# Kernel optimization log

Measured on AMD Instinct MI355X. Metric: run time of the kernel, lower is better.

## Reference

```python
import jax, jax.numpy as jnp
import numpy as np

RADIUS = 0.3      # extents/2, extents = radius_scale*6*particle_radius = 4*6*0.025 = 0.6
KSIZE = 4         # kernel_size [4,4,4]
KMAX = 80         # padded neighbor count
N = 50000
BOX = 5.2         # box side -> ~40 neighbors within RADIUS on average
CIN = 3
COUT = 3
_PI = 3.14159265358979323846


def _build_neighbors(pos, radius, kmax):
    # fixed-radius search (L2), ignore_query_point=True, padded to kmax per row
    n = pos.shape[0]
    r2 = radius * radius
    sq = (pos * pos).sum(1)
    idx = np.zeros((n, kmax), np.int32)
    msk = np.zeros((n, kmax), np.bool_)
    ch = 2500
    for s in range(0, n, ch):
        e = min(s + ch, n)
        d2 = sq[s:e, None] + sq[None, :] - 2.0 * (pos[s:e] @ pos.T)
        d2[np.arange(e - s), np.arange(s, e)] = np.inf  # radius_search_ignore_query_points
        rows, cols = np.nonzero(d2 < r2)
        starts = np.searchsorted(rows, np.arange(e - s))
        slot = np.arange(len(rows)) - starts[rows]
        keep = slot < kmax
        idx[rows[keep] + s, slot[keep]] = cols[keep]
        msk[rows[keep] + s, slot[keep]] = True
    return idx, msk


def setup_inputs():
    key = jax.random.key(0)
    k1, k2, k3 = jax.random.split(key, 3)
    pos = jax.random.uniform(k1, (N, 3), jnp.float32) * BOX
    vel = jax.random.normal(k2, (N, 3), jnp.float32)
    # keras 'uniform' initializer: U(-0.05, 0.05)
    kernel = jax.random.uniform(k3, (KSIZE, KSIZE, KSIZE, CIN, COUT), jnp.float32, -0.05, 0.05)
    nidx, nmask = _build_neighbors(np.asarray(pos), RADIUS, KMAX)
    return {"pos": pos, "vel": vel, "kernel": kernel,
            "neighbor_idx": jnp.asarray(nidx), "neighbor_mask": jnp.asarray(nmask)}


def _ball_to_cube_volume_preserving(u):
    # Open3D CoordinateTransformation.h: MapSphereToCylinder then MapCylinderToCube
    eps = 1e-12
    x, y, z = u[..., 0], u[..., 1], u[..., 2]
    sq = x * x + y * y + z * z
    norm = jnp.sqrt(jnp.maximum(sq, eps))
    sq_xy = x * x + y * y
    # sphere -> cylinder
    top = (1.25 * z * z) > sq_xy
    s_top = jnp.sqrt(3.0 * norm / (norm + jnp.abs(z)))
    s_side = norm / jnp.sqrt(jnp.maximum(sq_xy, eps))
    x1 = jnp.where(top, x * s_top, x * s_side)
    y1 = jnp.where(top, y * s_top, y * s_side)
    z1 = jnp.where(top, jnp.sign(z) * norm, 1.5 * z)
    small = sq < eps
    x1 = jnp.where(small, x, x1)
    y1 = jnp.where(small, y, y1)
    z1 = jnp.where(small, z, z1)
    # cylinder -> cube (equal-area disc->square on xy)
    sq_xy1 = x1 * x1 + y1 * y1
    norm_xy = jnp.sqrt(jnp.maximum(sq_xy1, eps))
    xbig = jnp.abs(y1) <= jnp.abs(x1)
    sx = jnp.sign(x1) * norm_xy
    sy = jnp.sign(y1) * norm_xy
    safe_x = jnp.where(jnp.abs(x1) > eps, x1, 1.0)
    safe_y = jnp.where(jnp.abs(y1) > eps, y1, 1.0)
    x2 = jnp.where(xbig, sx, sy * (4.0 / _PI) * jnp.arctan(x1 / safe_y))
    y2 = jnp.where(xbig, sx * (4.0 / _PI) * jnp.arctan(y1 / safe_x), sy)
    small_xy = sq_xy1 < eps
    x2 = jnp.where(small_xy, x1, x2)
    y2 = jnp.where(small_xy, y1, y2)
    return x2, y2, z1


def _grid_coords(c):
    # align_corners=True: [-1,1] -> [0, KSIZE-1]; 'linear' interpolation clamps to border
    t = jnp.clip((c + 1.0) * (0.5 * (KSIZE - 1)), 0.0, KSIZE - 1.0)
    t0 = jnp.floor(t)
    i0 = t0.astype(jnp.int32)
    i1 = jnp.minimum(i0 + 1, KSIZE - 1)
    f = t - t0
    return (i0, i1), (1.0 - f, f)


def _cconv(pos, vel, kernel, neighbor_idx, neighbor_mask):
    n = pos.shape[0]
    rel = pos[neighbor_idx] - pos[:, None, :]              # [N,K,3]
    d2 = jnp.sum(rel * rel, -1)
    # window_poly6 on squared distance normalized by radius^2
    imp = jnp.clip((1.0 - d2 / (RADIUS * RADIUS)) ** 3, 0.0, 1.0)
    imp = imp * neighbor_mask.astype(vel.dtype)
    cx, cy, cz = _ball_to_cube_volume_preserving(rel / RADIUS)
    (xi0, xi1), (wx0, wx1) = _grid_coords(cx)
    (yi0, yi1), (wy0, wy1) = _grid_coords(cy)
    (zi0, zi1), (wz0, wz1) = _grid_coords(cz)
    phi = vel[neighbor_idx] * imp[..., None]               # [N,K,Cin]
    rows = jnp.arange(n)[:, None]
    # accumulate window*trilinear-weighted features into the 64 filter taps,
    # then contract once with the flattened kernel (math identical to per-pair
    # interp(W) @ feat since everything is linear)
    A = jnp.zeros((n, KSIZE * KSIZE * KSIZE, vel.shape[1]), vel.dtype)
    for zi, wz in ((zi0, wz0), (zi1, wz1)):
        for yi, wy in ((yi0, wy0), (yi1, wy1)):
            for xi, wx in ((xi0, wx0), (xi1, wx1)):
                corner = (zi * KSIZE + yi) * KSIZE + xi
                A = A.at[rows, corner].add((wz * wy * wx)[..., None] * phi)
    Wflat = kernel.reshape(KSIZE * KSIZE * KSIZE, kernel.shape[3], kernel.shape[4])
    return jnp.einsum('ngi,gio->no', A, Wflat)        # [N, COUT]


def reference(pos, vel, kernel, neighbor_idx, neighbor_mask):
    return _cconv(pos, vel, kernel, neighbor_idx, neighbor_mask)
```

## Files before the change

kernel.cpp:

```cpp
#include <hip/hip_runtime.h>
#include <math.h>

#define N_PART 50000
#define KMAX 80
#define KS 4
#define LPP 16

typedef __attribute__((ext_vector_type(8))) _Float16 h8;
typedef __attribute__((ext_vector_type(2))) _Float16 h2;

__device__ __forceinline__ float atan_poly(float t) {
    float t2 = t * t;
    float p = -0.01172120f;
    p = p * t2 + 0.05265332f;
    p = p * t2 - 0.11643287f;
    p = p * t2 + 0.19354346f;
    p = p * t2 - 0.33262347f;
    p = p * t2 + 0.99997726f;
    return t * p;
}

template <typename MT>
__device__ __forceinline__ int prefix_count(const MT* __restrict__ nmask, int base, int sub) {
    int lc = 0; bool more = true;
    #pragma unroll
    for (int i = 0; i < 5; ++i) {
        bool t = nmask[base + sub * 5 + i] != 0;
        lc += (more && t) ? 1 : 0;
        more = more && t;
    }
    bool full = (lc == 5);
    unsigned long long nb = __ballot(!full);
    int wl  = threadIdx.x & 63;
    int grp = wl >> 4;
    unsigned int gb = (unsigned int)((nb >> (16 * grp)) & 0xFFFFull);
    if (gb == 0) return KMAX;
    int fi  = __ffs(gb) - 1;
    int flc = __shfl(lc, (grp << 4) + fi, 64);
    return fi * 5 + flc;
}

struct PV { float px, py, pz, ux, uy, uz; };

__device__ __forceinline__ void load_pv(const float* __restrict__ pos,
                                        const float* __restrict__ vel,
                                        int i, PV& v) {
    v.px = pos[3*i];  v.py = pos[3*i+1];  v.pz = pos[3*i+2];
    v.ux = vel[3*i];  v.uy = vel[3*i+1];  v.uz = vel[3*i+2];
}

__device__ __forceinline__ void pair_contrib(
    const PV& n, float cpx, float cpy, float cpz, float vmask,
    const _Float16* __restrict__ WsH, const float* __restrict__ Ws8,
    float& acc0, float& acc1, float& acc2)
{
    const float inv_r = 1.0f / 0.3f;
    const float eps   = 1e-12f;
    const float FOUR_OVER_PI = 1.27323954473516268615f;

    float rx = (n.px - cpx) * inv_r;
    float ry = (n.py - cpy) * inv_r;
    float rz = (n.pz - cpz) * inv_r;

    float sq = rx * rx + ry * ry + rz * rz;

    float t1  = 1.0f - sq;
    float imp = fminf(fmaxf(t1 * t1 * t1, 0.0f), 1.0f) * vmask;

    float norm  = sqrtf(fmaxf(sq, eps));
    float sq_xy = rx * rx + ry * ry;
    bool  top   = (1.25f * rz * rz) > sq_xy;
    float s_top  = sqrtf(3.0f * norm * __builtin_amdgcn_rcpf(norm + fabsf(rz)));
    float s_side = norm * __builtin_amdgcn_rsqf(fmaxf(sq_xy, eps));
    float s  = top ? s_top : s_side;
    float x1 = rx * s;
    float y1 = ry * s;
    float z1 = top ? copysignf(norm, rz) : 1.5f * rz;
    if (sq < eps) { x1 = rx; y1 = ry; z1 = rz; }

    float sq1 = x1 * x1 + y1 * y1;
    float nxy = sqrtf(fmaxf(sq1, eps));
    bool  xb  = fabsf(y1) <= fabsf(x1);
    float num = xb ? y1 : x1;
    float den = xb ? x1 : y1;
    float sden = (fabsf(den) > eps) ? den : 1.0f;
    float t    = num * __builtin_amdgcn_rcpf(sden);
    float at   = atan_poly(t);
    float sd   = copysignf(nxy, den);
    float u    = sd * FOUR_OVER_PI * at;
    float x2   = xb ? sd : u;
    float y2   = xb ? u  : sd;
    if (sq1 < eps) { x2 = x1; y2 = y1; }

    float tx = fminf(fmaxf((x2 + 1.0f) * 1.5f, 0.0f), 3.0f);
    float ty = fminf(fmaxf((y2 + 1.0f) * 1.5f, 0.0f), 3.0f);
    float tz = fminf(fmaxf((z1 + 1.0f) * 1.5f, 0.0f), 3.0f);
    float fx0 = floorf(tx), fy0 = floorf(ty), fz0 = floorf(tz);
    int xi0 = (int)fx0, yi0 = (int)fy0, zi0 = (int)fz0;
    int xi1 = min(xi0 + 1, KS - 1);
    int yi1 = min(yi0 + 1, KS - 1);
    int zi1 = min(zi0 + 1, KS - 1);
    float wx1 = tx - fx0, wx0 = 1.0f - wx1;
    float wy1 = ty - fy0, wy0 = 1.0f - wy1;
    float wz1 = tz - fz0, wz0 = 1.0f - wz1;

    int   zia[2] = { zi0, zi1 };  float wza[2] = { wz0, wz1 };
    int   yia[2] = { yi0, yi1 };  float wya[2] = { wy0, wy1 };
    int   xia[2] = { xi0, xi1 };  float wxa[2] = { wx0, wx1 };

    h2 M01 = (h2)(_Float16)0.0f;
    h2 M23 = (h2)(_Float16)0.0f;
    h2 M45 = (h2)(_Float16)0.0f;
    h2 M67 = (h2)(_Float16)0.0f;
    float m8 = 0.0f;

    #pragma unroll
    for (int cz = 0; cz < 2; ++cz) {
        #pragma unroll
        for (int cy = 0; cy < 2; ++cy) {
            float wzy = wza[cz] * wya[cy];
            #pragma unroll
            for (int cx = 0; cx < 2; ++cx) {
                int corner = (zia[cz] * KS + yia[cy]) * KS + xia[cx];
                h8 wv = *(const h8*)&WsH[corner << 3];
                float wf = wzy * wxa[cx];
                _Float16 wh = (_Float16)wf;
                h2 ww = { wh, wh };
                M01 += ww * __builtin_shufflevector(wv, wv, 0, 1);
                M23 += ww * __builtin_shufflevector(wv, wv, 2, 3);
                M45 += ww * __builtin_shufflevector(wv, wv, 4, 5);
                M67 += ww * __builtin_shufflevector(wv, wv, 6, 7);
                m8  += wf * Ws8[corner];
            }
        }
    }

    float m0 = (float)M01[0], m1 = (float)M01[1];
    float m2 = (float)M23[0], m3 = (float)M23[1];
    float m4 = (float)M45[0], m5 = (float)M45[1];
    float m6 = (float)M67[0], m7 = (float)M67[1];
    float s0 = n.ux * m0 + n.uy * m3 + n.uz * m6;
    float s1 = n.ux * m1 + n.uy * m4 + n.uz * m7;
    float s2 = n.ux * m2 + n.uy * m5 + n.uz * m8;
    acc0 += imp * s0;
    acc1 += imp * s1;
    acc2 += imp * s2;
}

__global__ __launch_bounds__(256) void cconv_kernel(
    const float* __restrict__ pos,
    const float* __restrict__ vel,
    const float* __restrict__ Wg,
    const int* __restrict__ nidx,
    const void* __restrict__ nmask,
    float* __restrict__ out)
{
    __shared__ _Float16 WsH[64 * 8];
    __shared__ float    Ws8[64];
    for (int t = threadIdx.x; t < 64 * 8; t += blockDim.x) {
        int g = t >> 3, r = t & 7;
        WsH[t] = (_Float16)Wg[g * 9 + r];
    }
    for (int t = threadIdx.x; t < 64; t += blockDim.x)
        Ws8[t] = Wg[t * 9 + 8];
    __syncthreads();

    int gid = blockIdx.x * blockDim.x + threadIdx.x;
    int p   = gid >> 4;
    int sub = gid & 15;
    if (p >= N_PART) return;

    const int base = p * KMAX;

    int idxs[5];
    #pragma unroll
    for (int m = 0; m < 5; ++m)
        idxs[m] = nidx[base + sub + (m << 4)];

    bool byteMask;
    {
        const unsigned* mw = (const unsigned*)nmask;
        int lane = threadIdx.x & 63;
        bool big = false;
        #pragma unroll
        for (int i = 0; i < 8; ++i)
            big |= (mw[lane + 64 * i] > 1u);
        byteMask = (__ballot(big) != 0ULL);
    }

    float cpx = pos[3 * p], cpy = pos[3 * p + 1], cpz = pos[3 * p + 2];

    int cnt;
    if (byteMask) cnt = prefix_count<unsigned char>((const unsigned char*)nmask, base, sub);
    else          cnt = prefix_count<int>((const int*)nmask, base, sub);

    int rem   = cnt - sub;
    int trips = (rem > 0) ? ((rem + 31) >> 5) : 0;

    PV A0, A1, A0n, A1n;
    load_pv(pos, vel, idxs[0], A0);
    load_pv(pos, vel, idxs[1], A1);

    float acc0 = 0.0f, acc1 = 0.0f, acc2 = 0.0f;

    for (int j = 0; j < trips; ++j) {
        int mn0 = min(2 * j + 2, 4);
        int mn1 = min(2 * j + 3, 4);
        load_pv(pos, vel, idxs[mn0], A0n);
        load_pv(pos, vel, idxs[mn1], A1n);

        int   k1 = sub + ((2 * j + 1) << 4);
        float v1 = (k1 < cnt) ? 1.0f : 0.0f;

        pair_contrib(A0, cpx, cpy, cpz, 1.0f, WsH, Ws8, acc0, acc1, acc2);
        pair_contrib(A1, cpx, cpy, cpz, v1,   WsH, Ws8, acc0, acc1, acc2);

        A0 = A0n; A1 = A1n;
    }

    acc0 += __shfl_xor(acc0, 1); acc0 += __shfl_xor(acc0, 2);
    acc0 += __shfl_xor(acc0, 4); acc0 += __shfl_xor(acc0, 8);
    acc1 += __shfl_xor(acc1, 1); acc1 += __shfl_xor(acc1, 2);
    acc1 += __shfl_xor(acc1, 4); acc1 += __shfl_xor(acc1, 8);
    acc2 += __shfl_xor(acc2, 1); acc2 += __shfl_xor(acc2, 2);
    acc2 += __shfl_xor(acc2, 4); acc2 += __shfl_xor(acc2, 8);

    if (sub == 0) {
        out[p * 3 + 0] = acc0;
        out[p * 3 + 1] = acc1;
        out[p * 3 + 2] = acc2;
    }
}

extern "C" void kernel_launch(void* const* d_in, const int* in_sizes, int n_in,
                              void* d_out, int out_size, void* d_ws, size_t ws_size,
                              hipStream_t stream) {
    const float* pos   = (const float*)d_in[0];
    const float* vel   = (const float*)d_in[1];
    const float* Wg    = (const float*)d_in[2];
    const int*   nidx  = (const int*)d_in[3];
    const void*  nmask = d_in[4];
    float*       out   = (float*)d_out;

    int threads = 256;
    long long total = (long long)N_PART * LPP;
    int grid = (int)((total + threads - 1) / threads);
    cconv_kernel<<<grid, threads, 0, stream>>>(pos, vel, Wg, nidx, nmask, out);
}
```

Measured before the change: 33.05 us.

## Parallelize over neighbor pairs with segmented wave reduction and atomics

Replaces the per-particle kernel (16 lanes looping over neighbors) with one thread per neighbor slot, reducing contributions per particle via a segmented shuffle scan within each wavefront and atomicAdd across wavefronts. A separate kernel zeroes the output first. This aims to expose more parallelism and drop the prefix-count loop, but it processes padded slots, adds a 6-step scan, atomics and an extra launch.

After: 51.25 us. +55.0%, slower.

```diff
diff --git a/kernel.cpp b/kernel.cpp
--- a/kernel.cpp
+++ b/kernel.cpp
@@ -4,7 +4,7 @@
 #define N_PART 50000
 #define KMAX 80
 #define KS 4
-#define LPP 16
+#define NTOT (N_PART * KMAX)
 
 typedef __attribute__((ext_vector_type(8))) _Float16 h8;
 typedef __attribute__((ext_vector_type(2))) _Float16 h2;
@@ -20,52 +20,69 @@
     return t * p;
 }
 
-template <typename MT>
-__device__ __forceinline__ int prefix_count(const MT* __restrict__ nmask, int base, int sub) {
-    int lc = 0; bool more = true;
-    #pragma unroll
-    for (int i = 0; i < 5; ++i) {
-        bool t = nmask[base + sub * 5 + i] != 0;
-        lc += (more && t) ? 1 : 0;
-        more = more && t;
-    }
-    bool full = (lc == 5);
-    unsigned long long nb = __ballot(!full);
-    int wl  = threadIdx.x & 63;
-    int grp = wl >> 4;
-    unsigned int gb = (unsigned int)((nb >> (16 * grp)) & 0xFFFFull);
-    if (gb == 0) return KMAX;
-    int fi  = __ffs(gb) - 1;
-    int flc = __shfl(lc, (grp << 4) + fi, 64);
-    return fi * 5 + flc;
-}
-
-struct PV { float px, py, pz, ux, uy, uz; };
-
-__device__ __forceinline__ void load_pv(const float* __restrict__ pos,
-                                        const float* __restrict__ vel,
-                                        int i, PV& v) {
-    v.px = pos[3*i];  v.py = pos[3*i+1];  v.pz = pos[3*i+2];
-    v.ux = vel[3*i];  v.uy = vel[3*i+1];  v.uz = vel[3*i+2];
-}
-
-__device__ __forceinline__ void pair_contrib(
-    const PV& n, float cpx, float cpy, float cpz, float vmask,
-    const _Float16* __restrict__ WsH, const float* __restrict__ Ws8,
-    float& acc0, float& acc1, float& acc2)
+__global__ __launch_bounds__(256) void zero_out_kernel(float* __restrict__ out, int n) {
+    int i = blockIdx.x * blockDim.x + threadIdx.x;
+    if (i < n) out[i] = 0.0f;
+}
+
+__global__ __launch_bounds__(256) void cconv_pair_kernel(
+    const float* __restrict__ pos,
+    const float* __restrict__ vel,
+    const float* __restrict__ Wg,
+    const int* __restrict__ nidx,
+    const void* __restrict__ nmask,
+    float* __restrict__ out)
 {
+    __shared__ _Float16 WsH[64 * 8];
+    __shared__ float    Ws8[64];
+    for (int t = threadIdx.x; t < 64 * 8; t += blockDim.x) {
+        int g = t >> 3, r = t & 7;
+        WsH[t] = (_Float16)Wg[g * 9 + r];
+    }
+    for (int t = threadIdx.x; t < 64; t += blockDim.x)
+        Ws8[t] = Wg[t * 9 + 8];
+    __syncthreads();
+
+    int t = blockIdx.x * blockDim.x + threadIdx.x;
+    unsigned tu = (unsigned)t;
+    int p    = (int)(tu / 80u);
+    int lane = threadIdx.x & 63;
+
+    bool byteMask;
+    {
+        const unsigned* mw = (const unsigned*)nmask;
+        bool big = false;
+        #pragma unroll
+        for (int i = 0; i < 8; ++i)
+            big |= (mw[lane + 64 * i] > 1u);
+        byteMask = (__ballot(big) != 0ULL);
+    }
+
+    bool valid;
+    if (byteMask) valid = ((const unsigned char*)nmask)[t] != 0;
+    else          valid = ((const int*)nmask)[t] != 0;
+
+    if (__ballot(valid) == 0ULL) return;
+
+    int   idx  = nidx[t];
+    float vmsk = valid ? 1.0f : 0.0f;
+
     const float inv_r = 1.0f / 0.3f;
     const float eps   = 1e-12f;
     const float FOUR_OVER_PI = 1.27323954473516268615f;
 
-    float rx = (n.px - cpx) * inv_r;
-    float ry = (n.py - cpy) * inv_r;
-    float rz = (n.pz - cpz) * inv_r;
+    float cpx = pos[3 * p], cpy = pos[3 * p + 1], cpz = pos[3 * p + 2];
+    float npx = pos[3 * idx], npy = pos[3 * idx + 1], npz = pos[3 * idx + 2];
+    float ux  = vel[3 * idx], uy  = vel[3 * idx + 1], uz  = vel[3 * idx + 2];
+
+    float rx = (npx - cpx) * inv_r;
+    float ry = (npy - cpy) * inv_r;
+    float rz = (npz - cpz) * inv_r;
 
     float sq = rx * rx + ry * ry + rz * rz;
 
     float t1  = 1.0f - sq;
-    float imp = fminf(fmaxf(t1 * t1 * t1, 0.0f), 1.0f) * vmask;
+    float imp = fminf(fmaxf(t1 * t1 * t1, 0.0f), 1.0f) * vmsk;
 
     float norm  = sqrtf(fmaxf(sq, eps));
     float sq_xy = rx * rx + ry * ry;
@@ -84,8 +101,8 @@
     float num = xb ? y1 : x1;
     float den = xb ? x1 : y1;
     float sden = (fabsf(den) > eps) ? den : 1.0f;
-    float t    = num * __builtin_amdgcn_rcpf(sden);
-    float at   = atan_poly(t);
+    float tt   = num * __builtin_amdgcn_rcpf(sden);
+    float at   = atan_poly(tt);
     float sd   = copysignf(nxy, den);
     float u    = sd * FOUR_OVER_PI * at;
     float x2   = xb ? sd : u;
@@ -139,96 +156,31 @@
     float m2 = (float)M23[0], m3 = (float)M23[1];
     float m4 = (float)M45[0], m5 = (float)M45[1];
     float m6 = (float)M67[0], m7 = (float)M67[1];
-    float s0 = n.ux * m0 + n.uy * m3 + n.uz * m6;
-    float s1 = n.ux * m1 + n.uy * m4 + n.uz * m7;
-    float s2 = n.ux * m2 + n.uy * m5 + n.uz * m8;
-    acc0 += imp * s0;
-    acc1 += imp * s1;
-    acc2 += imp * s2;
-}
-
-__global__ __launch_bounds__(256) void cconv_kernel(
-    const float* __restrict__ pos,
-    const float* __restrict__ vel,
-    const float* __restrict__ Wg,
-    const int* __restrict__ nidx,
-    const void* __restrict__ nmask,
-    float* __restrict__ out)
-{
-    __shared__ _Float16 WsH[64 * 8];
-    __shared__ float    Ws8[64];
-    for (int t = threadIdx.x; t < 64 * 8; t += blockDim.x) {
-        int g = t >> 3, r = t & 7;
-        WsH[t] = (_Float16)Wg[g * 9 + r];
-    }
-    for (int t = threadIdx.x; t < 64; t += blockDim.x)
-        Ws8[t] = Wg[t * 9 + 8];
-    __syncthreads();
-
-    int gid = blockIdx.x * blockDim.x + threadIdx.x;
-    int p   = gid >> 4;
-    int sub = gid & 15;
-    if (p >= N_PART) return;
-
-    const int base = p * KMAX;
-
-    int idxs[5];
+    float v0 = imp * (ux * m0 + uy * m3 + uz * m6);
+    float v1 = imp * (ux * m1 + uy * m4 + uz * m7);
+    float v2 = imp * (ux * m2 + uy * m5 + uz * m8);
+
     #pragma unroll
-    for (int m = 0; m < 5; ++m)
-        idxs[m] = nidx[base + sub + (m << 4)];
-
-    bool byteMask;
-    {
-        const unsigned* mw = (const unsigned*)nmask;
-        int lane = threadIdx.x & 63;
-        bool big = false;
-        #pragma unroll
-        for (int i = 0; i < 8; ++i)
-            big |= (mw[lane + 64 * i] > 1u);
-        byteMask = (__ballot(big) != 0ULL);
-    }
-
-    float cpx = pos[3 * p], cpy = pos[3 * p + 1], cpz = pos[3 * p + 2];
-
-    int cnt;
-    if (byteMask) cnt = prefix_count<unsigned char>((const unsigned char*)nmask, base, sub);
-    else          cnt = prefix_count<int>((const int*)nmask, base, sub);
-
-    int rem   = cnt - sub;
-    int trips = (rem > 0) ? ((rem + 31) >> 5) : 0;
-
-    PV A0, A1, A0n, A1n;
-    load_pv(pos, vel, idxs[0], A0);
-    load_pv(pos, vel, idxs[1], A1);
-
-    float acc0 = 0.0f, acc1 = 0.0f, acc2 = 0.0f;
-
-    for (int j = 0; j < trips; ++j) {
-        int mn0 = min(2 * j + 2, 4);
-        int mn1 = min(2 * j + 3, 4);
-        load_pv(pos, vel, idxs[mn0], A0n);
-        load_pv(pos, vel, idxs[mn1], A1n);
-
-        int   k1 = sub + ((2 * j + 1) << 4);
-        float v1 = (k1 < cnt) ? 1.0f : 0.0f;
-
-        pair_contrib(A0, cpx, cpy, cpz, 1.0f, WsH, Ws8, acc0, acc1, acc2);
-        pair_contrib(A1, cpx, cpy, cpz, v1,   WsH, Ws8, acc0, acc1, acc2);
-
-        A0 = A0n; A1 = A1n;
-    }
-
-    acc0 += __shfl_xor(acc0, 1); acc0 += __shfl_xor(acc0, 2);
-    acc0 += __shfl_xor(acc0, 4); acc0 += __shfl_xor(acc0, 8);
-    acc1 += __shfl_xor(acc1, 1); acc1 += __shfl_xor(acc1, 2);
-    acc1 += __shfl_xor(acc1, 4); acc1 += __shfl_xor(acc1, 8);
-    acc2 += __shfl_xor(acc2, 1); acc2 += __shfl_xor(acc2, 2);
-    acc2 += __shfl_xor(acc2, 4); acc2 += __shfl_xor(acc2, 8);
-
-    if (sub == 0) {
-        out[p * 3 + 0] = acc0;
-        out[p * 3 + 1] = acc1;
-        out[p * 3 + 2] = acc2;
+    for (int d = 1; d < 64; d <<= 1) {
+        int src = lane - d;
+        int cs  = max(src, 0);
+        int   pp = __shfl(p,  cs, 64);
+        float f0 = __shfl(v0, cs, 64);
+        float f1 = __shfl(v1, cs, 64);
+        float f2 = __shfl(v2, cs, 64);
+        bool take = (src >= 0) && (pp == p);
+        v0 += take ? f0 : 0.0f;
+        v1 += take ? f1 : 0.0f;
+        v2 += take ? f2 : 0.0f;
+    }
+
+    int  nl = min(lane + 1, 63);
+    int  pn = __shfl(p, nl, 64);
+    bool lastInSeg = (lane == 63) || (pn != p);
+    if (lastInSeg) {
+        atomicAdd(&out[3 * p + 0], v0);
+        atomicAdd(&out[3 * p + 1], v1);
+        atomicAdd(&out[3 * p + 2], v2);
     }
 }
 
@@ -242,8 +194,10 @@
     const void*  nmask = d_in[4];
     float*       out   = (float*)d_out;
 
+    int nOut = out_size;
+    zero_out_kernel<<<(nOut + 255) / 256, 256, 0, stream>>>(out, nOut);
+
     int threads = 256;
-    long long total = (long long)N_PART * LPP;
-    int grid = (int)((total + threads - 1) / threads);
-    cconv_kernel<<<grid, threads, 0, stream>>>(pos, vel, Wg, nidx, nmask, out);
-}
+    int grid    = NTOT / threads;
+    cconv_pair_kernel<<<grid, threads, 0, stream>>>(pos, vel, Wg, nidx, nmask, out);
+}
```

## Switch to persistent kernel with atomic work queues and simplify cylinder-norm math

Applied to the files above, without the earlier changes.

The kernel becomes persistent: 2048 blocks of waves pull quads of four particles from four partitioned atomic counters in the workspace, which is zeroed by a memset before launch. This is meant to balance uneven neighbor counts across waves and to cut block launch overhead. The weight staging into shared memory and the mask-format check now run once per wave instead of once per particle group. Separately, the cylinder radius nxy and the octant test are computed directly from existing values, dropping one sqrt and some arithmetic. The cost is an extra memset launch plus atomic traffic, and the ordering of work changes.

Measured after the change: 109.8 us. 3.32x slower.

```diff
diff --git a/kernel.cpp b/kernel.cpp
--- a/kernel.cpp
+++ b/kernel.cpp
@@ -4,7 +4,8 @@
 #define N_PART 50000
 #define KMAX 80
 #define KS 4
-#define LPP 16
+#define NQUAD 12500
+#define QPC 3125
 
 typedef __attribute__((ext_vector_type(8))) _Float16 h8;
 typedef __attribute__((ext_vector_type(2))) _Float16 h2;
@@ -67,22 +68,23 @@
     float t1  = 1.0f - sq;
     float imp = fminf(fmaxf(t1 * t1 * t1, 0.0f), 1.0f) * vmask;
 
-    float norm  = sqrtf(fmaxf(sq, eps));
-    float sq_xy = rx * rx + ry * ry;
-    bool  top   = (1.25f * rz * rz) > sq_xy;
+    float norm   = sqrtf(fmaxf(sq, eps));
+    float sq_xy  = rx * rx + ry * ry;
+    bool  top    = (1.25f * rz * rz) > sq_xy;
+    float rsq_xy = __builtin_amdgcn_rsqf(fmaxf(sq_xy, eps));
     float s_top  = sqrtf(3.0f * norm * __builtin_amdgcn_rcpf(norm + fabsf(rz)));
-    float s_side = norm * __builtin_amdgcn_rsqf(fmaxf(sq_xy, eps));
+    float s_side = norm * rsq_xy;
     float s  = top ? s_top : s_side;
     float x1 = rx * s;
     float y1 = ry * s;
     float z1 = top ? copysignf(norm, rz) : 1.5f * rz;
     if (sq < eps) { x1 = rx; y1 = ry; z1 = rz; }
 
-    float sq1 = x1 * x1 + y1 * y1;
-    float nxy = sqrtf(fmaxf(sq1, eps));
-    bool  xb  = fabsf(y1) <= fabsf(x1);
-    float num = xb ? y1 : x1;
-    float den = xb ? x1 : y1;
+    float nxy = top ? (sq_xy * rsq_xy * s_top) : norm;
+    float sq1 = nxy * nxy;
+    bool  xb  = fabsf(ry) <= fabsf(rx);
+    float num = xb ? ry : rx;
+    float den = xb ? rx : ry;
     float sden = (fabsf(den) > eps) ? den : 1.0f;
     float t    = num * __builtin_amdgcn_rcpf(sden);
     float at   = atan_poly(t);
@@ -147,12 +149,13 @@
     acc2 += imp * s2;
 }
 
-__global__ __launch_bounds__(256) void cconv_kernel(
+__global__ __launch_bounds__(256) void cconv_persist_kernel(
     const float* __restrict__ pos,
     const float* __restrict__ vel,
     const float* __restrict__ Wg,
     const int* __restrict__ nidx,
     const void* __restrict__ nmask,
+    int* __restrict__ ctrs,
     float* __restrict__ out)
 {
     __shared__ _Float16 WsH[64 * 8];
@@ -165,22 +168,13 @@
         Ws8[t] = Wg[t * 9 + 8];
     __syncthreads();
 
-    int gid = blockIdx.x * blockDim.x + threadIdx.x;
-    int p   = gid >> 4;
-    int sub = gid & 15;
-    if (p >= N_PART) return;
-
-    const int base = p * KMAX;
-
-    int idxs[5];
-    #pragma unroll
-    for (int m = 0; m < 5; ++m)
-        idxs[m] = nidx[base + sub + (m << 4)];
+    const int lane = threadIdx.x & 63;
+    const int sub  = lane & 15;
+    const int grp  = lane >> 4;
 
     bool byteMask;
     {
         const unsigned* mw = (const unsigned*)nmask;
-        int lane = threadIdx.x & 63;
         bool big = false;
         #pragma unroll
         for (int i = 0; i < 8; ++i)
@@ -188,47 +182,66 @@
         byteMask = (__ballot(big) != 0ULL);
     }
 
-    float cpx = pos[3 * p], cpy = pos[3 * p + 1], cpz = pos[3 * p + 2];
-
-    int cnt;
-    if (byteMask) cnt = prefix_count<unsigned char>((const unsigned char*)nmask, base, sub);
-    else          cnt = prefix_count<int>((const int*)nmask, base, sub);
-
-    int rem   = cnt - sub;
-    int trips = (rem > 0) ? ((rem + 31) >> 5) : 0;
-
-    PV A0, A1, A0n, A1n;
-    load_pv(pos, vel, idxs[0], A0);
-    load_pv(pos, vel, idxs[1], A1);
-
-    float acc0 = 0.0f, acc1 = 0.0f, acc2 = 0.0f;
-
-    for (int j = 0; j < trips; ++j) {
-        int mn0 = min(2 * j + 2, 4);
-        int mn1 = min(2 * j + 3, 4);
-        load_pv(pos, vel, idxs[mn0], A0n);
-        load_pv(pos, vel, idxs[mn1], A1n);
-
-        int   k1 = sub + ((2 * j + 1) << 4);
-        float v1 = (k1 < cnt) ? 1.0f : 0.0f;
-
-        pair_contrib(A0, cpx, cpy, cpz, 1.0f, WsH, Ws8, acc0, acc1, acc2);
-        pair_contrib(A1, cpx, cpy, cpz, v1,   WsH, Ws8, acc0, acc1, acc2);
-
-        A0 = A0n; A1 = A1n;
-    }
-
-    acc0 += __shfl_xor(acc0, 1); acc0 += __shfl_xor(acc0, 2);
-    acc0 += __shfl_xor(acc0, 4); acc0 += __shfl_xor(acc0, 8);
-    acc1 += __shfl_xor(acc1, 1); acc1 += __shfl_xor(acc1, 2);
-    acc1 += __shfl_xor(acc1, 4); acc1 += __shfl_xor(acc1, 8);
-    acc2 += __shfl_xor(acc2, 1); acc2 += __shfl_xor(acc2, 2);
-    acc2 += __shfl_xor(acc2, 4); acc2 += __shfl_xor(acc2, 8);
-
-    if (sub == 0) {
-        out[p * 3 + 0] = acc0;
-        out[p * 3 + 1] = acc1;
-        out[p * 3 + 2] = acc2;
+    const int gwave = blockIdx.x * (blockDim.x >> 6) + (threadIdx.x >> 6);
+    const int part  = gwave & 3;
+    int* myctr = ctrs + part * 16;
+
+    for (;;) {
+        int q;
+        if (lane == 0) q = atomicAdd(myctr, 1);
+        q = __shfl(q, 0, 64);
+        if (q >= QPC) break;
+
+        const int p    = ((part * QPC + q) << 2) + grp;
+        const int base = p * KMAX;
+
+        int idxs[5];
+        #pragma unroll
+        for (int m = 0; m < 5; ++m)
+            idxs[m] = nidx[base + sub + (m << 4)];
+
+        float cpx = pos[3 * p], cpy = pos[3 * p + 1], cpz = pos[3 * p + 2];
+
+        int cnt;
+        if (byteMask) cnt = prefix_count<unsigned char>((const unsigned char*)nmask, base, sub);
+        else          cnt = prefix_count<int>((const int*)nmask, base, sub);
+
+        int rem   = cnt - sub;
+        int trips = (rem > 0) ? ((rem + 31) >> 5) : 0;
+
+        PV A0, A1, A0n, A1n;
+        load_pv(pos, vel, idxs[0], A0);
+        load_pv(pos, vel, idxs[1], A1);
+
+        float acc0 = 0.0f, acc1 = 0.0f, acc2 = 0.0f;
+
+        for (int j = 0; j < trips; ++j) {
+            int mn0 = min(2 * j + 2, 4);
+            int mn1 = min(2 * j + 3, 4);
+            load_pv(pos, vel, idxs[mn0], A0n);
+            load_pv(pos, vel, idxs[mn1], A1n);
+
+            int   k1 = sub + ((2 * j + 1) << 4);
+            float v1 = (k1 < cnt) ? 1.0f : 0.0f;
+
+            pair_contrib(A0, cpx, cpy, cpz, 1.0f, WsH, Ws8, acc0, acc1, acc2);
+            pair_contrib(A1, cpx, cpy, cpz, v1,   WsH, Ws8, acc0, acc1, acc2);
+
+            A0 = A0n; A1 = A1n;
+        }
+
+        acc0 += __shfl_xor(acc0, 1); acc0 += __shfl_xor(acc0, 2);
+        acc0 += __shfl_xor(acc0, 4); acc0 += __shfl_xor(acc0, 8);
+        acc1 += __shfl_xor(acc1, 1); acc1 += __shfl_xor(acc1, 2);
+        acc1 += __shfl_xor(acc1, 4); acc1 += __shfl_xor(acc1, 8);
+        acc2 += __shfl_xor(acc2, 1); acc2 += __shfl_xor(acc2, 2);
+        acc2 += __shfl_xor(acc2, 4); acc2 += __shfl_xor(acc2, 8);
+
+        if (sub == 0) {
+            out[p * 3 + 0] = acc0;
+            out[p * 3 + 1] = acc1;
+            out[p * 3 + 2] = acc2;
+        }
     }
 }
 
@@ -241,9 +254,9 @@
     const int*   nidx  = (const int*)d_in[3];
     const void*  nmask = d_in[4];
     float*       out   = (float*)d_out;
-
-    int threads = 256;
-    long long total = (long long)N_PART * LPP;
-    int grid = (int)((total + threads - 1) / threads);
-    cconv_kernel<<<grid, threads, 0, stream>>>(pos, vel, Wg, nidx, nmask, out);
-}
+    int*         ctrs  = (int*)d_ws;
+
+    hipMemsetAsync(d_ws, 0, 256, stream);
+
+    cconv_persist_kernel<<<2048, 256, 0, stream>>>(pos, vel, Wg, nidx, nmask, ctrs, out);
+}
```

## Simplify ball-to-cube math and switch to single-pair neighbor loop

Applied to the files above, without the earlier changes.

Drops the redundant eps-guarded branches and clamps in the pair computation. The cylinder-to-cube step now works directly on rx/ry with an analytically derived xy norm, because the cylinder scaling keeps the xy direction. Corner index arithmetic is strength-reduced with pre-shifted indices. The neighbor loop goes from processing two pairs per iteration with a validity mask to one pair per iteration bounded by the count, which removes wasted masked work but gives up some ILP.

Result: faster. 29.16 us (-11.8%).

```diff
diff --git a/kernel.cpp b/kernel.cpp
--- a/kernel.cpp
+++ b/kernel.cpp
@@ -50,7 +50,7 @@
 }
 
 __device__ __forceinline__ void pair_contrib(
-    const PV& n, float cpx, float cpy, float cpz, float vmask,
+    const PV& n, float cpx, float cpy, float cpz,
     const _Float16* __restrict__ WsH, const float* __restrict__ Ws8,
     float& acc0, float& acc1, float& acc2)
 {
@@ -65,24 +65,21 @@
     float sq = rx * rx + ry * ry + rz * rz;
 
     float t1  = 1.0f - sq;
-    float imp = fminf(fmaxf(t1 * t1 * t1, 0.0f), 1.0f) * vmask;
-
-    float norm  = sqrtf(fmaxf(sq, eps));
-    float sq_xy = rx * rx + ry * ry;
-    bool  top   = (1.25f * rz * rz) > sq_xy;
+    float imp = fmaxf(t1 * t1 * t1, 0.0f);
+
+    float norm   = sqrtf(fmaxf(sq, eps));
+    float sq_xy  = rx * rx + ry * ry;
+    bool  top    = (1.25f * rz * rz) > sq_xy;
+    float rsq_xy = __builtin_amdgcn_rsqf(fmaxf(sq_xy, eps));
     float s_top  = sqrtf(3.0f * norm * __builtin_amdgcn_rcpf(norm + fabsf(rz)));
-    float s_side = norm * __builtin_amdgcn_rsqf(fmaxf(sq_xy, eps));
+    float s_side = norm * rsq_xy;
     float s  = top ? s_top : s_side;
-    float x1 = rx * s;
-    float y1 = ry * s;
     float z1 = top ? copysignf(norm, rz) : 1.5f * rz;
-    if (sq < eps) { x1 = rx; y1 = ry; z1 = rz; }
-
-    float sq1 = x1 * x1 + y1 * y1;
-    float nxy = sqrtf(fmaxf(sq1, eps));
-    bool  xb  = fabsf(y1) <= fabsf(x1);
-    float num = xb ? y1 : x1;
-    float den = xb ? x1 : y1;
+
+    float nxy = top ? (sq_xy * rsq_xy * s_top) : norm;
+    bool  xb  = fabsf(ry) <= fabsf(rx);
+    float num = xb ? ry : rx;
+    float den = xb ? rx : ry;
     float sden = (fabsf(den) > eps) ? den : 1.0f;
     float t    = num * __builtin_amdgcn_rcpf(sden);
     float at   = atan_poly(t);
@@ -90,7 +87,6 @@
     float u    = sd * FOUR_OVER_PI * at;
     float x2   = xb ? sd : u;
     float y2   = xb ? u  : sd;
-    if (sq1 < eps) { x2 = x1; y2 = y1; }
 
     float tx = fminf(fmaxf((x2 + 1.0f) * 1.5f, 0.0f), 3.0f);
     float ty = fminf(fmaxf((y2 + 1.0f) * 1.5f, 0.0f), 3.0f);
@@ -104,9 +100,9 @@
     float wy1 = ty - fy0, wy0 = 1.0f - wy1;
     float wz1 = tz - fz0, wz0 = 1.0f - wz1;
 
-    int   zia[2] = { zi0, zi1 };  float wza[2] = { wz0, wz1 };
-    int   yia[2] = { yi0, yi1 };  float wya[2] = { wy0, wy1 };
-    int   xia[2] = { xi0, xi1 };  float wxa[2] = { wx0, wx1 };
+    int   zia[2] = { zi0 << 4, zi1 << 4 };  float wza[2] = { wz0, wz1 };
+    int   yia[2] = { yi0 << 2, yi1 << 2 };  float wya[2] = { wy0, wy1 };
+    int   xia[2] = { xi0, xi1 };            float wxa[2] = { wx0, wx1 };
 
     h2 M01 = (h2)(_Float16)0.0f;
     h2 M23 = (h2)(_Float16)0.0f;
@@ -119,9 +115,10 @@
         #pragma unroll
         for (int cy = 0; cy < 2; ++cy) {
             float wzy = wza[cz] * wya[cy];
+            int   czy = zia[cz] + yia[cy];
             #pragma unroll
             for (int cx = 0; cx < 2; ++cx) {
-                int corner = (zia[cz] * KS + yia[cy]) * KS + xia[cx];
+                int corner = czy + xia[cx];
                 h8 wv = *(const h8*)&WsH[corner << 3];
                 float wf = wzy * wxa[cx];
                 _Float16 wh = (_Float16)wf;
@@ -194,28 +191,19 @@
     if (byteMask) cnt = prefix_count<unsigned char>((const unsigned char*)nmask, base, sub);
     else          cnt = prefix_count<int>((const int*)nmask, base, sub);
 
-    int rem   = cnt - sub;
-    int trips = (rem > 0) ? ((rem + 31) >> 5) : 0;
-
-    PV A0, A1, A0n, A1n;
-    load_pv(pos, vel, idxs[0], A0);
-    load_pv(pos, vel, idxs[1], A1);
+    PV A, An;
+    load_pv(pos, vel, idxs[0], A);
 
     float acc0 = 0.0f, acc1 = 0.0f, acc2 = 0.0f;
 
-    for (int j = 0; j < trips; ++j) {
-        int mn0 = min(2 * j + 2, 4);
-        int mn1 = min(2 * j + 3, 4);
-        load_pv(pos, vel, idxs[mn0], A0n);
-        load_pv(pos, vel, idxs[mn1], A1n);
-
-        int   k1 = sub + ((2 * j + 1) << 4);
-        float v1 = (k1 < cnt) ? 1.0f : 0.0f;
-
-        pair_contrib(A0, cpx, cpy, cpz, 1.0f, WsH, Ws8, acc0, acc1, acc2);
-        pair_contrib(A1, cpx, cpy, cpz, v1,   WsH, Ws8, acc0, acc1, acc2);
-
-        A0 = A0n; A1 = A1n;
+    int m = 0;
+    for (int k = sub; k < cnt; k += LPP) {
+        int mn = min(m + 1, 4);
+        load_pv(pos, vel, idxs[mn], An);
+
+        pair_contrib(A, cpx, cpy, cpz, WsH, Ws8, acc0, acc1, acc2);
+
+        A = An; ++m;
     }
 
     acc0 += __shfl_xor(acc0, 1); acc0 += __shfl_xor(acc0, 2);
```
